# Kernel optimization log

Measured on AMD Instinct MI355X. Metric: run time of the kernel, lower is better.

## Reference

```python
import jax, jax.numpy as jnp
import numpy as np

N_NODES = 50000
N_EDGES = 600000
NUM_RELS = 5
IN_CH = 768
HID = 128
OUT_CH = 128
REL_DIM = 200


def _segment_softmax(scores, seg, n):
    # numerically stable softmax over variable-size segments (destination nodes)
    m = jax.ops.segment_max(scores, seg, num_segments=n)
    e = jnp.exp(scores - m[seg])
    s = jax.ops.segment_sum(e, seg, num_segments=n)
    return e / s[seg]


def _hgn_conv(x, edge_index, edge_type, W, Wr, a, Wres, rel_tab, final):
    # x: [N, h_in]; W: [h, h_in]; Wr: [h, rel_dim]; a: [3h]; rel_tab: [R, rel_dim]
    src = edge_index[0]
    dst = edge_index[1]
    n = x.shape[0]
    h = W.shape[0]
    Wx = x @ W.T                      # [N, h] (shared by x_i, x_j, messages)
    rel = rel_tab[edge_type] @ Wr.T   # [E, h]
    aA, aB, aC = a[:h], a[h:2 * h], a[2 * h:]
    # a([Wx_i | Wx_j | Wr rel]) decomposed to avoid materializing the concat
    score = Wx[dst] @ aA + Wx[src] @ aB + rel @ aC   # [E]
    alpha = jax.nn.leaky_relu(score, 0.2)
    alpha = _segment_softmax(alpha, dst, n)
    agg = jax.ops.segment_sum(Wx[src] * alpha[:, None], dst, num_segments=n)
    out = jax.nn.elu(agg + x @ Wres.T)
    if final:
        out = out / jnp.maximum(jnp.linalg.norm(out, axis=1, keepdims=True), 1e-12)
    return out, alpha


def setup_inputs() -> dict:
    key = jax.random.key(0)
    ks = jax.random.split(key, 20)
    s = 0.02
    return {
        "x": jax.random.normal(ks[0], (N_NODES, IN_CH), jnp.float32),
        "edge_index": jax.random.randint(ks[1], (2, N_EDGES), 0, N_NODES, jnp.int64 if jax.config.jax_enable_x64 else jnp.int32),
        "edge_type": jax.random.randint(ks[2], (N_EDGES,), 0, NUM_RELS, jnp.int64 if jax.config.jax_enable_x64 else jnp.int32),
        "l1_W": jax.random.normal(ks[3], (HID, IN_CH), jnp.float32) * s,
        "l1_b": jnp.zeros((HID,), jnp.float32),
        "l2_W": jax.random.normal(ks[4], (OUT_CH, HID), jnp.float32) * s,
        "l2_b": jnp.zeros((OUT_CH,), jnp.float32),
        "W1": jax.random.normal(ks[5], (HID, HID), jnp.float32) * s,
        "Wr1": jax.random.normal(ks[6], (HID, REL_DIM), jnp.float32) * s,
        "a1": jax.random.normal(ks[7], (3 * HID,), jnp.float32) * s,
        "Wres1": jax.random.normal(ks[8], (HID, HID), jnp.float32) * s,
        "rel1": jax.random.normal(ks[9], (NUM_RELS, REL_DIM), jnp.float32),
        "W2": jax.random.normal(ks[10], (HID, HID), jnp.float32) * s,
        "Wr2": jax.random.normal(ks[11], (HID, REL_DIM), jnp.float32) * s,
        "a2": jax.random.normal(ks[12], (3 * HID,), jnp.float32) * s,
        "Wres2": jax.random.normal(ks[13], (HID, HID), jnp.float32) * s,
        "rel2": jax.random.normal(ks[14], (NUM_RELS, REL_DIM), jnp.float32),
    }


def reference(x, edge_index, edge_type, l1_W, l1_b, l2_W, l2_b,
              W1, Wr1, a1, Wres1, rel1, W2, Wr2, a2, Wres2, rel2):
    out = jax.nn.leaky_relu(x @ l1_W.T + l1_b, 0.01)
    # layer 1 (dropout is identity in eval mode)
    out, alpha = _hgn_conv(out, edge_index, edge_type, W1, Wr1, a1, Wres1, rel1, final=False)
    # layer 2: original code blends alpha into self.alpha but weights messages
    # with its own (unblended) softmax alpha, so pre_alpha does not affect output
    out, _ = _hgn_conv(out, edge_index, edge_type, W2, Wr2, a2, Wres2, rel2, final=True)
    out = jax.nn.leaky_relu(out @ l2_W.T + l2_b, 0.01)
    return out
```

## Files before the change

### kernel.cpp

```cpp
#include <hip/hip_runtime.h>

namespace {

typedef unsigned short ushort_t;
typedef unsigned int uint_t;
typedef __attribute__((ext_vector_type(8))) short bf16x8;
typedef __attribute__((ext_vector_type(4))) float f32x4;

constexpr int N   = 50000;
constexpr int E   = 600000;
constexpr int NR  = 5;
constexpr int KIN = 768;
constexpr int H   = 128;
constexpr int RD  = 200;

__device__ inline ushort_t f2b(float f){
  uint_t u = __builtin_bit_cast(uint_t, f);
  uint_t r = (u + 0x7FFFu + ((u >> 16) & 1u)) >> 16;
  return (ushort_t)r;
}
__device__ inline float b2f_lo(uint_t u){ return __builtin_bit_cast(float, u << 16); }
__device__ inline float b2f_hi(uint_t u){ return __builtin_bit_cast(float, u & 0xFFFF0000u); }

__global__ void cvt_all_k(const float* __restrict__ l1W, const float* __restrict__ W1,
                          const float* __restrict__ R1, const float* __restrict__ W2,
                          const float* __restrict__ R2, const float* __restrict__ l2W,
                          ushort_t* __restrict__ dst){
  constexpr int S0 = H * KIN;
  constexpr int S1 = H * H;
  int i = blockIdx.x * 256 + threadIdx.x;
  if (i >= S0 + 5 * S1) return;
  float v;
  if (i < S0) v = l1W[i];
  else {
    int j = i - S0, seg = j >> 14, off = j & (S1 - 1);
    const float* srcs[5] = {W1, R1, W2, R2, l2W};
    v = srcs[seg][off];
  }
  dst[i] = f2b(v);
}

__global__ void relsc_k(const float* __restrict__ rel1, const float* __restrict__ Wr1,
                        const float* __restrict__ a1, float* __restrict__ sC1,
                        const float* __restrict__ rel2, const float* __restrict__ Wr2,
                        const float* __restrict__ a2, float* __restrict__ sC2){
  const float* rel = blockIdx.x ? rel2 : rel1;
  const float* Wr  = blockIdx.x ? Wr2  : Wr1;
  const float* a   = blockIdx.x ? a2   : a1;
  float*       sC  = blockIdx.x ? sC2  : sC1;
  __shared__ float red[128];
  int n = threadIdx.x;
  float aC = a[256 + n];
  for (int r = 0; r < NR; ++r){
    float p = 0.f;
    for (int k = 0; k < RD; ++k) p += rel[r * RD + k] * Wr[n * RD + k];
    red[n] = p * aC;
    __syncthreads();
    for (int s = 64; s > 0; s >>= 1){
      if (n < s) red[n] += red[n + s];
      __syncthreads();
    }
    if (n == 0) sC[r] = red[0];
    __syncthreads();
  }
}

template<int K, int MODE, bool AFP32, bool OUTBF, bool NORM>
__global__ __launch_bounds__(256) void mgemm_k(const void* __restrict__ Ap,
    const ushort_t* __restrict__ Wb, const float* __restrict__ avec,
    const float* __restrict__ aggM, void* __restrict__ outp,
    float* __restrict__ sA, float* __restrict__ sB, int M)
{
  constexpr int AP = 40;
  constexpr int BP = 40;
  __shared__ __align__(16) ushort_t As[64 * AP];
  __shared__ __align__(16) ushort_t Bs[128 * BP];
  const int tid  = threadIdx.x;
  const int wave = tid >> 6, lane = tid & 63;
  const int l15  = lane & 15, quad = lane >> 4;
  const int row0 = blockIdx.x * 64;

  f32x4 acc[8];
  #pragma unroll
  for (int t = 0; t < 8; ++t) acc[t] = (f32x4){0.f, 0.f, 0.f, 0.f};

  for (int k0 = 0; k0 < K; k0 += 32){
    {
      int r = tid >> 2, q = tid & 3;
      int grow = row0 + r;
      ushort_t v[8] = {0,0,0,0,0,0,0,0};
      if (grow < M){
        if (AFP32){
          const float* ap = (const float*)Ap + (size_t)grow * K + k0 + q * 8;
          float4 u0 = *reinterpret_cast<const float4*>(ap);
          float4 u1 = *reinterpret_cast<const float4*>(ap + 4);
          v[0]=f2b(u0.x); v[1]=f2b(u0.y); v[2]=f2b(u0.z); v[3]=f2b(u0.w);
          v[4]=f2b(u1.x); v[5]=f2b(u1.y); v[6]=f2b(u1.z); v[7]=f2b(u1.w);
        } else {
          const uint4 u = *reinterpret_cast<const uint4*>(
              (const ushort_t*)Ap + (size_t)grow * K + k0 + q * 8);
          *reinterpret_cast<uint4*>(v) = u;
        }
      }
      *reinterpret_cast<uint4*>(&As[r * AP + q * 8]) = *reinterpret_cast<uint4*>(v);
    }
    {
      int n = tid >> 1, seg = tid & 1;
      const ushort_t* wp = Wb + (size_t)n * K + k0 + seg * 16;
      uint4 v0 = *reinterpret_cast<const uint4*>(wp);
      uint4 v1 = *reinterpret_cast<const uint4*>(wp + 8);
      *reinterpret_cast<uint4*>(&Bs[n * BP + seg * 16])     = v0;
      *reinterpret_cast<uint4*>(&Bs[n * BP + seg * 16 + 8]) = v1;
    }
    __syncthreads();
    bf16x8 af = *reinterpret_cast<const bf16x8*>(&As[(wave * 16 + l15) * AP + quad * 8]);
    #pragma unroll
    for (int t = 0; t < 8; ++t){
      bf16x8 bf = *reinterpret_cast<const bf16x8*>(&Bs[(t * 16 + l15) * BP + quad * 8]);
      acc[t] = __builtin_amdgcn_mfma_f32_16x16x32_bf16(af, bf, acc[t], 0, 0, 0);
    }
    __syncthreads();
  }

  float vv[8][4];
  #pragma unroll
  for (int t = 0; t < 8; ++t){
    #pragma unroll
    for (int r = 0; r < 4; ++r){
      int grow = row0 + wave * 16 + quad * 4 + r;
      int col  = t * 16 + l15;
      float v = acc[t][r];
      if (MODE == 1){
        v += avec[col];
        v = v > 0.f ? v : 0.01f * v;
      } else if (MODE == 2){
        if (grow < M) v += aggM[(size_t)grow * 128 + col];
        v = v > 0.f ? v : __expf(v) - 1.f;
      }
      vv[t][r] = v;
    }
  }

  if (MODE == 3){
    #pragma unroll
    for (int r = 0; r < 4; ++r){
      float pa = 0.f, pb = 0.f;
      #pragma unroll
      for (int t = 0; t < 8; ++t){
        int col = t * 16 + l15;
        pa += vv[t][r] * avec[col];
        pb += vv[t][r] * avec[128 + col];
      }
      #pragma unroll
      for (int off = 1; off < 16; off <<= 1){
        pa += __shfl_xor(pa, off, 64);
        pb += __shfl_xor(pb, off, 64);
      }
      int grow = row0 + wave * 16 + quad * 4 + r;
      if (l15 == r && grow < M){ sA[grow] = pa; sB[grow] = pb; }
    }
  }

  if (NORM){
    #pragma unroll
    for (int r = 0; r < 4; ++r){
      float ss = 0.f;
      #pragma unroll
      for (int t = 0; t < 8; ++t) ss += vv[t][r] * vv[t][r];
      #pragma unroll
      for (int off = 1; off < 16; off <<= 1) ss += __shfl_xor(ss, off, 64);
      float sc = 1.f / fmaxf(sqrtf(ss), 1e-12f);
      #pragma unroll
      for (int t = 0; t < 8; ++t) vv[t][r] *= sc;
    }
  }

  #pragma unroll
  for (int t = 0; t < 8; ++t){
    #pragma unroll
    for (int r = 0; r < 4; ++r){
      int grow = row0 + wave * 16 + quad * 4 + r;
      if (grow >= M) continue;
      int col = t * 16 + l15;
      if (OUTBF) ((ushort_t*)outp)[(size_t)grow * 128 + col] = f2b(vv[t][r]);
      else       ((float*)outp)   [(size_t)grow * 128 + col] = vv[t][r];
    }
  }
}

__global__ void degcount_k(const int* __restrict__ dst, int* __restrict__ deg){
  int e = blockIdx.x * 256 + threadIdx.x;
  if (e < E) atomicAdd(&deg[dst[e]], 1);
}

__global__ void scan1_k(const int* __restrict__ deg, int* __restrict__ chunk,
                        int* __restrict__ bsums, int n){
  __shared__ int s[256];
  int tid = threadIdx.x, i = blockIdx.x * 256 + tid;
  int v = (i < n) ? deg[i] : 0;
  s[tid] = v; __syncthreads();
  for (int off = 1; off < 256; off <<= 1){
    int t = (tid >= off) ? s[tid - off] : 0;
    __syncthreads();
    s[tid] += t;
    __syncthreads();
  }
  if (i < n) chunk[i] = s[tid] - v;
  if (tid == 255) bsums[blockIdx.x] = s[255];
}

__global__ void scan2_k(const int* __restrict__ bsums, int* __restrict__ boffs, int nb){
  __shared__ int s[256];
  int tid = threadIdx.x;
  int v = (tid < nb) ? bsums[tid] : 0;
  s[tid] = v; __syncthreads();
  for (int off = 1; off < 256; off <<= 1){
    int t = (tid >= off) ? s[tid - off] : 0;
    __syncthreads();
    s[tid] += t;
    __syncthreads();
  }
  if (tid < nb) boffs[tid] = s[tid] - v;
}

__global__ void scan3_k(int* __restrict__ rowptr, const int* __restrict__ boffs,
                        int* __restrict__ cursor, int n, int total){
  int i = blockIdx.x * 256 + threadIdx.x;
  if (i < n){
    int v = rowptr[i] + boffs[blockIdx.x];
    rowptr[i] = v; cursor[i] = v;
  }
  if (i == 0) rowptr[n] = total;
}

__global__ void fill_k(const int* __restrict__ src, const int* __restrict__ dst,
                       const int* __restrict__ et, int* __restrict__ cursor,
                       int* __restrict__ csrc, int* __restrict__ ctype){
  int e = blockIdx.x * 256 + threadIdx.x;
  if (e < E){
    int d = dst[e];
    int p = atomicAdd(&cursor[d], 1);
    csrc[p]  = src[e];
    ctype[p] = et[e];
  }
}

__global__ void agg_k(const ushort_t* __restrict__ Wx, const float* __restrict__ sA,
                      const float* __restrict__ sB, const float* __restrict__ sC,
                      const int* __restrict__ rowptr, const int* __restrict__ csrc,
                      const int* __restrict__ ctype, float* __restrict__ agg, int n){
  int node = blockIdx.x * 4 + (threadIdx.x >> 6);
  int lane = threadIdx.x & 63;
  if (node >= n) return;
  int p0 = rowptr[node], p1 = rowptr[node + 1];
  int deg = p1 - p0;
  float sa = sA[node];
  float m = -1e30f, ssum = 0.f, a0 = 0.f, a1 = 0.f;

  for (int c0 = 0; c0 < deg; c0 += 64){
    int cnt = deg - c0; if (cnt > 64) cnt = 64;
    bool ok = lane < cnt;
    int p = p0 + c0 + (ok ? lane : 0);
    int sn = csrc[p];
    int tp = ctype[p];
    float s = sa + sB[sn] + sC[tp];
    s = s > 0.f ? s : 0.2f * s;
    float sv = ok ? s : -1e30f;
    #pragma unroll
    for (int off = 32; off > 0; off >>= 1) sv = fmaxf(sv, __shfl_xor(sv, off, 64));
    float mn = fmaxf(m, sv);
    float corr = __expf(m - mn);
    ssum *= corr; a0 *= corr; a1 *= corr;
    float ev = ok ? __expf(s - mn) : 0.f;
    float es = ev;
    #pragma unroll
    for (int off = 32; off > 0; off >>= 1) es += __shfl_xor(es, off, 64);
    ssum += es;
    int sng = ok ? sn : 0;
    m = mn;

    for (int e = 0; e < cnt; e += 4){
      int  n0 = __shfl(sng, e,     64), n1 = __shfl(sng, e + 1, 64);
      int  n2 = __shfl(sng, e + 2, 64), n3 = __shfl(sng, e + 3, 64);
      float e0 = __shfl(ev, e,     64), e1 = __shfl(ev, e + 1, 64);
      float e2 = __shfl(ev, e + 2, 64), e3 = __shfl(ev, e + 3, 64);
      uint_t u0 = *reinterpret_cast<const uint_t*>(Wx + (size_t)n0 * 128 + lane * 2);
      uint_t u1 = *reinterpret_cast<const uint_t*>(Wx + (size_t)n1 * 128 + lane * 2);
      uint_t u2 = *reinterpret_cast<const uint_t*>(Wx + (size_t)n2 * 128 + lane * 2);
      uint_t u3 = *reinterpret_cast<const uint_t*>(Wx + (size_t)n3 * 128 + lane * 2);
      a0 += e0 * b2f_lo(u0); a1 += e0 * b2f_hi(u0);
      a0 += e1 * b2f_lo(u1); a1 += e1 * b2f_hi(u1);
      a0 += e2 * b2f_lo(u2); a1 += e2 * b2f_hi(u2);
      a0 += e3 * b2f_lo(u3); a1 += e3 * b2f_hi(u3);
    }
  }
  float inv = (deg > 0) ? 1.f / ssum : 0.f;
  float2 w; w.x = a0 * inv; w.y = a1 * inv;
  *reinterpret_cast<float2*>(agg + (size_t)node * 128 + lane * 2) = w;
}

}

extern "C" void kernel_launch(void* const* d_in, const int* in_sizes, int n_in,
                              void* d_out, int out_size, void* d_ws, size_t ws_size,
                              hipStream_t stream)
{
  const float* x     = (const float*)d_in[0];
  const int*   eidx  = (const int*)d_in[1];
  const int*   et    = (const int*)d_in[2];
  const float* l1W   = (const float*)d_in[3];
  const float* l1b   = (const float*)d_in[4];
  const float* l2W   = (const float*)d_in[5];
  const float* l2b   = (const float*)d_in[6];
  const float* W1    = (const float*)d_in[7];
  const float* Wr1   = (const float*)d_in[8];
  const float* a1    = (const float*)d_in[9];
  const float* Wres1 = (const float*)d_in[10];
  const float* rel1  = (const float*)d_in[11];
  const float* W2    = (const float*)d_in[12];
  const float* Wr2   = (const float*)d_in[13];
  const float* a2    = (const float*)d_in[14];
  const float* Wres2 = (const float*)d_in[15];
  const float* rel2  = (const float*)d_in[16];
  float* outp = (float*)d_out;

  const int* esrc = eidx;
  const int* edst = eidx + E;

  float* f = (float*)d_ws;
  size_t o = 0;
  float* aggF = f + o; o += (size_t)N * H;
  float* sA   = f + o; o += N;
  float* sB   = f + o; o += N;
  float* sC1  = f + o; o += 8;
  float* sC2  = f + o; o += 8;
  ushort_t* us = (ushort_t*)(f + o);
  size_t ou = 0;
  ushort_t* b0   = us + ou; ou += (size_t)N * H;
  ushort_t* b1   = us + ou; ou += (size_t)N * H;
  ushort_t* Wxb  = us + ou; ou += (size_t)N * H;
  ushort_t* wtsb = us + ou; ou += (size_t)H * KIN + 5 * H * H;
  ushort_t* l1Wb = wtsb;
  ushort_t* W1b  = wtsb + H * KIN;
  ushort_t* R1b  = W1b + H * H;
  ushort_t* W2b  = R1b + H * H;
  ushort_t* R2b  = W2b + H * H;
  ushort_t* l2Wb = R2b + H * H;
  if (ou & 1) ou += 1;
  int* wi = (int*)(us + ou);
  size_t oi = 0;
  int* deg    = wi + oi; oi += N;
  int* rowptr = wi + oi; oi += N + 1;
  int* cursor = wi + oi; oi += N;
  int* bsums  = wi + oi; oi += 256;
  int* boffs  = wi + oi; oi += 256;
  int* csrc   = wi + oi; oi += E;
  int* ctype  = wi + oi; oi += E;

  const int EB    = (E + 255) / 256;
  const int NB256 = (N + 255) / 256;
  const int GB    = (N + 63) / 64;
  const int NB4   = (N + 3) / 4;
  const int CVB   = (H * KIN + 5 * H * H + 255) / 256;

  hipMemsetAsync(deg, 0, sizeof(int) * N, stream);
  degcount_k<<<EB, 256, 0, stream>>>(edst, deg);
  scan1_k<<<NB256, 256, 0, stream>>>(deg, rowptr, bsums, N);
  scan2_k<<<1, 256, 0, stream>>>(bsums, boffs, NB256);
  scan3_k<<<NB256, 256, 0, stream>>>(rowptr, boffs, cursor, N, E);
  fill_k<<<EB, 256, 0, stream>>>(esrc, edst, et, cursor, csrc, ctype);

  cvt_all_k<<<CVB, 256, 0, stream>>>(l1W, W1, Wres1, W2, Wres2, l2W, wtsb);
  relsc_k<<<2, 128, 0, stream>>>(rel1, Wr1, a1, sC1, rel2, Wr2, a2, sC2);

  mgemm_k<KIN, 1, true, true, false><<<GB, 256, 0, stream>>>(
      x, l1Wb, l1b, nullptr, b0, nullptr, nullptr, N);

  mgemm_k<H, 3, false, true, false><<<GB, 256, 0, stream>>>(
      b0, W1b, a1, nullptr, Wxb, sA, sB, N);
  agg_k<<<NB4, 256, 0, stream>>>(Wxb, sA, sB, sC1, rowptr, csrc, ctype, aggF, N);
  mgemm_k<H, 2, false, true, false><<<GB, 256, 0, stream>>>(
      b0, R1b, nullptr, aggF, b1, nullptr, nullptr, N);

  mgemm_k<H, 3, false, true, false><<<GB, 256, 0, stream>>>(
      b1, W2b, a2, nullptr, Wxb, sA, sB, N);
  agg_k<<<NB4, 256, 0, stream>>>(Wxb, sA, sB, sC2, rowptr, csrc, ctype, aggF, N);
  mgemm_k<H, 2, false, true, true><<<GB, 256, 0, stream>>>(
      b1, R2b, nullptr, aggF, b0, nullptr, nullptr, N);

  mgemm_k<H, 1, false, false, false><<<GB, 256, 0, stream>>>(
      b0, l2Wb, l2b, nullptr, outp, nullptr, nullptr, N);
}
```

Baseline: 529.1 us.

## Fuse consecutive GEMMs per row block, pack edge CSR, bf16 aggregation buffer

Chains each pair of consecutive per-node GEMMs into one kernel: the first GEMM's epilogue output is kept in shared memory as bf16 and fed straight into the second GEMM, so the intermediate no longer needs a global round trip or a separate launch. Edge source and type are packed into one int in the CSR, and the aggregation output becomes bf16 instead of fp32, which cuts memory traffic. The weight conversion, degree zeroing and relation-score setup are merged into one prep kernel. In exchange it uses more shared memory per block, adds extra bf16 rounding of the aggregate, and the 16-bit source packing only works while node ids stay below 65536.

```diff
diff --git a/kernel.cpp b/kernel.cpp
--- a/kernel.cpp
+++ b/kernel.cpp
@@ -21,169 +21,53 @@
 }
 __device__ inline float b2f_lo(uint_t u){ return __builtin_bit_cast(float, u << 16); }
 __device__ inline float b2f_hi(uint_t u){ return __builtin_bit_cast(float, u & 0xFFFF0000u); }
-
-__global__ void cvt_all_k(const float* __restrict__ l1W, const float* __restrict__ W1,
-                          const float* __restrict__ R1, const float* __restrict__ W2,
-                          const float* __restrict__ R2, const float* __restrict__ l2W,
-                          ushort_t* __restrict__ dst){
+__device__ inline float b2f_us(ushort_t h){ return __builtin_bit_cast(float, ((uint_t)h) << 16); }
+
+__global__ void prep_k(const float* __restrict__ l1W, const float* __restrict__ W1,
+                       const float* __restrict__ R1, const float* __restrict__ W2,
+                       const float* __restrict__ R2, const float* __restrict__ l2W,
+                       ushort_t* __restrict__ wts, int* __restrict__ deg,
+                       const float* __restrict__ rel1, const float* __restrict__ Wr1,
+                       const float* __restrict__ a1, float* __restrict__ sC1,
+                       const float* __restrict__ rel2, const float* __restrict__ Wr2,
+                       const float* __restrict__ a2, float* __restrict__ sC2){
   constexpr int S0 = H * KIN;
   constexpr int S1 = H * H;
-  int i = blockIdx.x * 256 + threadIdx.x;
-  if (i >= S0 + 5 * S1) return;
-  float v;
-  if (i < S0) v = l1W[i];
-  else {
-    int j = i - S0, seg = j >> 14, off = j & (S1 - 1);
-    const float* srcs[5] = {W1, R1, W2, R2, l2W};
-    v = srcs[seg][off];
-  }
-  dst[i] = f2b(v);
-}
-
-__global__ void relsc_k(const float* __restrict__ rel1, const float* __restrict__ Wr1,
-                        const float* __restrict__ a1, float* __restrict__ sC1,
-                        const float* __restrict__ rel2, const float* __restrict__ Wr2,
-                        const float* __restrict__ a2, float* __restrict__ sC2){
-  const float* rel = blockIdx.x ? rel2 : rel1;
-  const float* Wr  = blockIdx.x ? Wr2  : Wr1;
-  const float* a   = blockIdx.x ? a2   : a1;
-  float*       sC  = blockIdx.x ? sC2  : sC1;
-  __shared__ float red[128];
-  int n = threadIdx.x;
-  float aC = a[256 + n];
-  for (int r = 0; r < NR; ++r){
-    float p = 0.f;
-    for (int k = 0; k < RD; ++k) p += rel[r * RD + k] * Wr[n * RD + k];
-    red[n] = p * aC;
-    __syncthreads();
-    for (int s = 64; s > 0; s >>= 1){
-      if (n < s) red[n] += red[n + s];
+  int b = blockIdx.x, tid = threadIdx.x;
+  if (b < 704){
+    int i = b * 256 + tid;
+    float v;
+    if (i < S0) v = l1W[i];
+    else {
+      int j = i - S0, seg = j >> 14, off = j & (S1 - 1);
+      const float* srcs[5] = {W1, R1, W2, R2, l2W};
+      v = srcs[seg][off];
+    }
+    wts[i] = f2b(v);
+  } else if (b < 900){
+    int i = (b - 704) * 256 + tid;
+    if (i < N) deg[i] = 0;
+  } else {
+    int L = b - 900;
+    const float* rel = L ? rel2 : rel1;
+    const float* Wr  = L ? Wr2  : Wr1;
+    const float* a   = L ? a2   : a1;
+    float*       sC  = L ? sC2  : sC1;
+    __shared__ float red[256];
+    int n = tid >> 1, half = tid & 1;
+    float aC = a[256 + n];
+    for (int r = 0; r < NR; ++r){
+      float p = 0.f;
+      for (int k = half * 100; k < half * 100 + 100; ++k)
+        p += rel[r * RD + k] * Wr[n * RD + k];
+      red[tid] = p * aC;
       __syncthreads();
-    }
-    if (n == 0) sC[r] = red[0];
-    __syncthreads();
-  }
-}
-
-template<int K, int MODE, bool AFP32, bool OUTBF, bool NORM>
-__global__ __launch_bounds__(256) void mgemm_k(const void* __restrict__ Ap,
-    const ushort_t* __restrict__ Wb, const float* __restrict__ avec,
-    const float* __restrict__ aggM, void* __restrict__ outp,
-    float* __restrict__ sA, float* __restrict__ sB, int M)
-{
-  constexpr int AP = 40;
-  constexpr int BP = 40;
-  __shared__ __align__(16) ushort_t As[64 * AP];
-  __shared__ __align__(16) ushort_t Bs[128 * BP];
-  const int tid  = threadIdx.x;
-  const int wave = tid >> 6, lane = tid & 63;
-  const int l15  = lane & 15, quad = lane >> 4;
-  const int row0 = blockIdx.x * 64;
-
-  f32x4 acc[8];
-  #pragma unroll
-  for (int t = 0; t < 8; ++t) acc[t] = (f32x4){0.f, 0.f, 0.f, 0.f};
-
-  for (int k0 = 0; k0 < K; k0 += 32){
-    {
-      int r = tid >> 2, q = tid & 3;
-      int grow = row0 + r;
-      ushort_t v[8] = {0,0,0,0,0,0,0,0};
-      if (grow < M){
-        if (AFP32){
-          const float* ap = (const float*)Ap + (size_t)grow * K + k0 + q * 8;
-          float4 u0 = *reinterpret_cast<const float4*>(ap);
-          float4 u1 = *reinterpret_cast<const float4*>(ap + 4);
-          v[0]=f2b(u0.x); v[1]=f2b(u0.y); v[2]=f2b(u0.z); v[3]=f2b(u0.w);
-          v[4]=f2b(u1.x); v[5]=f2b(u1.y); v[6]=f2b(u1.z); v[7]=f2b(u1.w);
-        } else {
-          const uint4 u = *reinterpret_cast<const uint4*>(
-              (const ushort_t*)Ap + (size_t)grow * K + k0 + q * 8);
-          *reinterpret_cast<uint4*>(v) = u;
-        }
-      }
-      *reinterpret_cast<uint4*>(&As[r * AP + q * 8]) = *reinterpret_cast<uint4*>(v);
-    }
-    {
-      int n = tid >> 1, seg = tid & 1;
-      const ushort_t* wp = Wb + (size_t)n * K + k0 + seg * 16;
-      uint4 v0 = *reinterpret_cast<const uint4*>(wp);
-      uint4 v1 = *reinterpret_cast<const uint4*>(wp + 8);
-      *reinterpret_cast<uint4*>(&Bs[n * BP + seg * 16])     = v0;
-      *reinterpret_cast<uint4*>(&Bs[n * BP + seg * 16 + 8]) = v1;
-    }
-    __syncthreads();
-    bf16x8 af = *reinterpret_cast<const bf16x8*>(&As[(wave * 16 + l15) * AP + quad * 8]);
-    #pragma unroll
-    for (int t = 0; t < 8; ++t){
-      bf16x8 bf = *reinterpret_cast<const bf16x8*>(&Bs[(t * 16 + l15) * BP + quad * 8]);
-      acc[t] = __builtin_amdgcn_mfma_f32_16x16x32_bf16(af, bf, acc[t], 0, 0, 0);
-    }
-    __syncthreads();
-  }
-
-  float vv[8][4];
-  #pragma unroll
-  for (int t = 0; t < 8; ++t){
-    #pragma unroll
-    for (int r = 0; r < 4; ++r){
-      int grow = row0 + wave * 16 + quad * 4 + r;
-      int col  = t * 16 + l15;
-      float v = acc[t][r];
-      if (MODE == 1){
-        v += avec[col];
-        v = v > 0.f ? v : 0.01f * v;
-      } else if (MODE == 2){
-        if (grow < M) v += aggM[(size_t)grow * 128 + col];
-        v = v > 0.f ? v : __expf(v) - 1.f;
-      }
-      vv[t][r] = v;
-    }
-  }
-
-  if (MODE == 3){
-    #pragma unroll
-    for (int r = 0; r < 4; ++r){
-      float pa = 0.f, pb = 0.f;
-      #pragma unroll
-      for (int t = 0; t < 8; ++t){
-        int col = t * 16 + l15;
-        pa += vv[t][r] * avec[col];
-        pb += vv[t][r] * avec[128 + col];
-      }
-      #pragma unroll
-      for (int off = 1; off < 16; off <<= 1){
-        pa += __shfl_xor(pa, off, 64);
-        pb += __shfl_xor(pb, off, 64);
-      }
-      int grow = row0 + wave * 16 + quad * 4 + r;
-      if (l15 == r && grow < M){ sA[grow] = pa; sB[grow] = pb; }
-    }
-  }
-
-  if (NORM){
-    #pragma unroll
-    for (int r = 0; r < 4; ++r){
-      float ss = 0.f;
-      #pragma unroll
-      for (int t = 0; t < 8; ++t) ss += vv[t][r] * vv[t][r];
-      #pragma unroll
-      for (int off = 1; off < 16; off <<= 1) ss += __shfl_xor(ss, off, 64);
-      float sc = 1.f / fmaxf(sqrtf(ss), 1e-12f);
-      #pragma unroll
-      for (int t = 0; t < 8; ++t) vv[t][r] *= sc;
-    }
-  }
-
-  #pragma unroll
-  for (int t = 0; t < 8; ++t){
-    #pragma unroll
-    for (int r = 0; r < 4; ++r){
-      int grow = row0 + wave * 16 + quad * 4 + r;
-      if (grow >= M) continue;
-      int col = t * 16 + l15;
-      if (OUTBF) ((ushort_t*)outp)[(size_t)grow * 128 + col] = f2b(vv[t][r]);
-      else       ((float*)outp)   [(size_t)grow * 128 + col] = vv[t][r];
+      for (int s = 128; s > 0; s >>= 1){
+        if (tid < s) red[tid] += red[tid + s];
+        __syncthreads();
+      }
+      if (tid == 0) sC[r] = red[0];
+      __syncthreads();
     }
   }
 }
@@ -235,20 +119,202 @@
 
 __global__ void fill_k(const int* __restrict__ src, const int* __restrict__ dst,
                        const int* __restrict__ et, int* __restrict__ cursor,
-                       int* __restrict__ csrc, int* __restrict__ ctype){
+                       int* __restrict__ cpk){
   int e = blockIdx.x * 256 + threadIdx.x;
   if (e < E){
     int d = dst[e];
     int p = atomicAdd(&cursor[d], 1);
-    csrc[p]  = src[e];
-    ctype[p] = et[e];
+    cpk[p] = src[e] | (et[e] << 16);
+  }
+}
+
+template<int K1, int M1, bool AFP32, bool NORM, bool STORE1, int M2>
+__global__ __launch_bounds__(256) void gfused_k(
+    const void* __restrict__ Ap, const ushort_t* __restrict__ Wb1,
+    const float* __restrict__ bias1, const ushort_t* __restrict__ aggM,
+    ushort_t* __restrict__ out1,
+    const ushort_t* __restrict__ Wb2, const float* __restrict__ vec2,
+    void* __restrict__ out2, float* __restrict__ sA, float* __restrict__ sB, int M)
+{
+  constexpr int AP = 40;
+  constexpr int BP = 40;
+  constexpr int CP = 136;
+  __shared__ __align__(16) ushort_t As[64 * AP];
+  __shared__ __align__(16) ushort_t Bs[128 * BP];
+  __shared__ __align__(16) ushort_t Cs[64 * CP];
+  const int tid  = threadIdx.x;
+  const int wave = tid >> 6, lane = tid & 63;
+  const int l15  = lane & 15, quad = lane >> 4;
+  const int row0 = blockIdx.x * 64;
+
+  if (M1 == 2){
+    #pragma unroll
+    for (int i = 0; i < 4; ++i){
+      int idx = tid + 256 * i;
+      int r = idx >> 4, c8 = idx & 15;
+      int grow = row0 + r;
+      uint4 v = make_uint4(0, 0, 0, 0);
+      if (grow < M) v = *reinterpret_cast<const uint4*>(aggM + (size_t)grow * 128 + c8 * 8);
+      *reinterpret_cast<uint4*>(&Cs[r * CP + c8 * 8]) = v;
+    }
+  }
+
+  f32x4 acc[8];
+  #pragma unroll
+  for (int t = 0; t < 8; ++t) acc[t] = (f32x4){0.f, 0.f, 0.f, 0.f};
+
+  for (int k0 = 0; k0 < K1; k0 += 32){
+    {
+      int r = tid >> 2, q = tid & 3;
+      int grow = row0 + r;
+      ushort_t v[8] = {0,0,0,0,0,0,0,0};
+      if (grow < M){
+        if (AFP32){
+          const float* ap = (const float*)Ap + (size_t)grow * K1 + k0 + q * 8;
+          float4 u0 = *reinterpret_cast<const float4*>(ap);
+          float4 u1 = *reinterpret_cast<const float4*>(ap + 4);
+          v[0]=f2b(u0.x); v[1]=f2b(u0.y); v[2]=f2b(u0.z); v[3]=f2b(u0.w);
+          v[4]=f2b(u1.x); v[5]=f2b(u1.y); v[6]=f2b(u1.z); v[7]=f2b(u1.w);
+        } else {
+          const uint4 u = *reinterpret_cast<const uint4*>(
+              (const ushort_t*)Ap + (size_t)grow * K1 + k0 + q * 8);
+          *reinterpret_cast<uint4*>(v) = u;
+        }
+      }
+      *reinterpret_cast<uint4*>(&As[r * AP + q * 8]) = *reinterpret_cast<uint4*>(v);
+    }
+    {
+      int n = tid >> 1, seg = tid & 1;
+      const ushort_t* wp = Wb1 + (size_t)n * K1 + k0 + seg * 16;
+      uint4 v0 = *reinterpret_cast<const uint4*>(wp);
+      uint4 v1 = *reinterpret_cast<const uint4*>(wp + 8);
+      *reinterpret_cast<uint4*>(&Bs[n * BP + seg * 16])     = v0;
+      *reinterpret_cast<uint4*>(&Bs[n * BP + seg * 16 + 8]) = v1;
+    }
+    __syncthreads();
+    bf16x8 af = *reinterpret_cast<const bf16x8*>(&As[(wave * 16 + l15) * AP + quad * 8]);
+    #pragma unroll
+    for (int t = 0; t < 8; ++t){
+      bf16x8 bfr = *reinterpret_cast<const bf16x8*>(&Bs[(t * 16 + l15) * BP + quad * 8]);
+      acc[t] = __builtin_amdgcn_mfma_f32_16x16x32_bf16(af, bfr, acc[t], 0, 0, 0);
+    }
+    __syncthreads();
+  }
+
+  float vv[8][4];
+  #pragma unroll
+  for (int t = 0; t < 8; ++t){
+    #pragma unroll
+    for (int r = 0; r < 4; ++r){
+      int lr  = wave * 16 + quad * 4 + r;
+      int col = t * 16 + l15;
+      float v = acc[t][r];
+      if (M1 == 1){
+        v += bias1[col];
+        v = v > 0.f ? v : 0.01f * v;
+      } else {
+        v += b2f_us(Cs[lr * CP + col]);
+        v = v > 0.f ? v : __expf(v) - 1.f;
+      }
+      vv[t][r] = v;
+    }
+  }
+  if (NORM){
+    #pragma unroll
+    for (int r = 0; r < 4; ++r){
+      float ss = 0.f;
+      #pragma unroll
+      for (int t = 0; t < 8; ++t) ss += vv[t][r] * vv[t][r];
+      #pragma unroll
+      for (int off = 1; off < 16; off <<= 1) ss += __shfl_xor(ss, off, 64);
+      float sc = 1.f / fmaxf(sqrtf(ss), 1e-12f);
+      #pragma unroll
+      for (int t = 0; t < 8; ++t) vv[t][r] *= sc;
+    }
+  }
+  #pragma unroll
+  for (int t = 0; t < 8; ++t){
+    #pragma unroll
+    for (int r = 0; r < 4; ++r){
+      int lr  = wave * 16 + quad * 4 + r;
+      int col = t * 16 + l15;
+      int grow = row0 + lr;
+      ushort_t h = f2b(vv[t][r]);
+      if (STORE1 && grow < M) out1[(size_t)grow * 128 + col] = h;
+      Cs[lr * CP + col] = h;
+    }
+  }
+  __syncthreads();
+
+  #pragma unroll
+  for (int t = 0; t < 8; ++t) acc[t] = (f32x4){0.f, 0.f, 0.f, 0.f};
+  for (int k0 = 0; k0 < 128; k0 += 32){
+    {
+      int n = tid >> 1, seg = tid & 1;
+      const ushort_t* wp = Wb2 + (size_t)n * 128 + k0 + seg * 16;
+      uint4 v0 = *reinterpret_cast<const uint4*>(wp);
+      uint4 v1 = *reinterpret_cast<const uint4*>(wp + 8);
+      *reinterpret_cast<uint4*>(&Bs[n * BP + seg * 16])     = v0;
+      *reinterpret_cast<uint4*>(&Bs[n * BP + seg * 16 + 8]) = v1;
+    }
+    __syncthreads();
+    bf16x8 af = *reinterpret_cast<const bf16x8*>(&Cs[(wave * 16 + l15) * CP + k0 + quad * 8]);
+    #pragma unroll
+    for (int t = 0; t < 8; ++t){
+      bf16x8 bfr = *reinterpret_cast<const bf16x8*>(&Bs[(t * 16 + l15) * BP + quad * 8]);
+      acc[t] = __builtin_amdgcn_mfma_f32_16x16x32_bf16(af, bfr, acc[t], 0, 0, 0);
+    }
+    __syncthreads();
+  }
+
+  if (M2 == 1){
+    #pragma unroll
+    for (int t = 0; t < 8; ++t){
+      #pragma unroll
+      for (int r = 0; r < 4; ++r){
+        int grow = row0 + wave * 16 + quad * 4 + r;
+        if (grow >= M) continue;
+        int col = t * 16 + l15;
+        float v = acc[t][r] + vec2[col];
+        v = v > 0.f ? v : 0.01f * v;
+        ((float*)out2)[(size_t)grow * 128 + col] = v;
+      }
+    }
+  } else {
+    #pragma unroll
+    for (int t = 0; t < 8; ++t){
+      #pragma unroll
+      for (int r = 0; r < 4; ++r){
+        int grow = row0 + wave * 16 + quad * 4 + r;
+        if (grow >= M) continue;
+        int col = t * 16 + l15;
+        ((ushort_t*)out2)[(size_t)grow * 128 + col] = f2b(acc[t][r]);
+      }
+    }
+    #pragma unroll
+    for (int r = 0; r < 4; ++r){
+      float pa = 0.f, pb = 0.f;
+      #pragma unroll
+      for (int t = 0; t < 8; ++t){
+        int col = t * 16 + l15;
+        pa += acc[t][r] * vec2[col];
+        pb += acc[t][r] * vec2[128 + col];
+      }
+      #pragma unroll
+      for (int off = 1; off < 16; off <<= 1){
+        pa += __shfl_xor(pa, off, 64);
+        pb += __shfl_xor(pb, off, 64);
+      }
+      int grow = row0 + wave * 16 + quad * 4 + r;
+      if (l15 == r && grow < M){ sA[grow] = pa; sB[grow] = pb; }
+    }
   }
 }
 
 __global__ void agg_k(const ushort_t* __restrict__ Wx, const float* __restrict__ sA,
                       const float* __restrict__ sB, const float* __restrict__ sC,
-                      const int* __restrict__ rowptr, const int* __restrict__ csrc,
-                      const int* __restrict__ ctype, float* __restrict__ agg, int n){
+                      const int* __restrict__ rowptr, const int* __restrict__ cpk,
+                      uint_t* __restrict__ aggU, int n){
   int node = blockIdx.x * 4 + (threadIdx.x >> 6);
   int lane = threadIdx.x & 63;
   if (node >= n) return;
@@ -260,10 +326,10 @@
   for (int c0 = 0; c0 < deg; c0 += 64){
     int cnt = deg - c0; if (cnt > 64) cnt = 64;
     bool ok = lane < cnt;
-    int p = p0 + c0 + (ok ? lane : 0);
-    int sn = csrc[p];
-    int tp = ctype[p];
-    float s = sa + sB[sn] + sC[tp];
+    int p  = p0 + c0 + (ok ? lane : 0);
+    int pk = cpk[p];
+    int sn = pk & 0xFFFF;
+    float s = sa + sB[sn] + sC[pk >> 16];
     s = s > 0.f ? s : 0.2f * s;
     float sv = ok ? s : -1e30f;
     #pragma unroll
@@ -276,12 +342,12 @@
     #pragma unroll
     for (int off = 32; off > 0; off >>= 1) es += __shfl_xor(es, off, 64);
     ssum += es;
-    int sng = ok ? sn : 0;
+    int png = ok ? pk : 0;
     m = mn;
 
     for (int e = 0; e < cnt; e += 4){
-      int  n0 = __shfl(sng, e,     64), n1 = __shfl(sng, e + 1, 64);
-      int  n2 = __shfl(sng, e + 2, 64), n3 = __shfl(sng, e + 3, 64);
+      int  n0 = __shfl(png, e,     64) & 0xFFFF, n1 = __shfl(png, e + 1, 64) & 0xFFFF;
+      int  n2 = __shfl(png, e + 2, 64) & 0xFFFF, n3 = __shfl(png, e + 3, 64) & 0xFFFF;
       float e0 = __shfl(ev, e,     64), e1 = __shfl(ev, e + 1, 64);
       float e2 = __shfl(ev, e + 2, 64), e3 = __shfl(ev, e + 3, 64);
       uint_t u0 = *reinterpret_cast<const uint_t*>(Wx + (size_t)n0 * 128 + lane * 2);
@@ -295,8 +361,8 @@
     }
   }
   float inv = (deg > 0) ? 1.f / ssum : 0.f;
-  float2 w; w.x = a0 * inv; w.y = a1 * inv;
-  *reinterpret_cast<float2*>(agg + (size_t)node * 128 + lane * 2) = w;
+  uint_t o = (uint_t)f2b(a0 * inv) | ((uint_t)f2b(a1 * inv) << 16);
+  aggU[(size_t)node * 64 + lane] = o;
 }
 
 }
@@ -329,7 +395,6 @@
 
   float* f = (float*)d_ws;
   size_t o = 0;
-  float* aggF = f + o; o += (size_t)N * H;
   float* sA   = f + o; o += N;
   float* sB   = f + o; o += N;
   float* sC1  = f + o; o += 8;
@@ -339,6 +404,7 @@
   ushort_t* b0   = us + ou; ou += (size_t)N * H;
   ushort_t* b1   = us + ou; ou += (size_t)N * H;
   ushort_t* Wxb  = us + ou; ou += (size_t)N * H;
+  ushort_t* aggB = us + ou; ou += (size_t)N * H;
   ushort_t* wtsb = us + ou; ou += (size_t)H * KIN + 5 * H * H;
   ushort_t* l1Wb = wtsb;
   ushort_t* W1b  = wtsb + H * KIN;
@@ -354,40 +420,29 @@
   int* cursor = wi + oi; oi += N;
   int* bsums  = wi + oi; oi += 256;
   int* boffs  = wi + oi; oi += 256;
-  int* csrc   = wi + oi; oi += E;
-  int* ctype  = wi + oi; oi += E;
+  int* cpk    = wi + oi; oi += E;
 
   const int EB    = (E + 255) / 256;
   const int NB256 = (N + 255) / 256;
   const int GB    = (N + 63) / 64;
   const int NB4   = (N + 3) / 4;
-  const int CVB   = (H * KIN + 5 * H * H + 255) / 256;
-
-  hipMemsetAsync(deg, 0, sizeof(int) * N, stream);
+
+  prep_k<<<902, 256, 0, stream>>>(l1W, W1, Wres1, W2, Wres2, l2W, wtsb, deg,
+                                  rel1, Wr1, a1, sC1, rel2, Wr2, a2, sC2);
   degcount_k<<<EB, 256, 0, stream>>>(edst, deg);
   scan1_k<<<NB256, 256, 0, stream>>>(deg, rowptr, bsums, N);
   scan2_k<<<1, 256, 0, stream>>>(bsums, boffs, NB256);
   scan3_k<<<NB256, 256, 0, stream>>>(rowptr, boffs, cursor, N, E);
-  fill_k<<<EB, 256, 0, stream>>>(esrc, edst, et, cursor, csrc, ctype);
-
-  cvt_all_k<<<CVB, 256, 0, stream>>>(l1W, W1, Wres1, W2, Wres2, l2W, wtsb);
-  relsc_k<<<2, 128, 0, stream>>>(rel1, Wr1, a1, sC1, rel2, Wr2, a2, sC2);
-
-  mgemm_k<KIN, 1, true, true, false><<<GB, 256, 0, stream>>>(
-      x, l1Wb, l1b, nullptr, b0, nullptr, nullptr, N);
-
-  mgemm_k<H, 3, false, true, false><<<GB, 256, 0, stream>>>(
-      b0, W1b, a1, nullptr, Wxb, sA, sB, N);
-  agg_k<<<NB4, 256, 0, stream>>>(Wxb, sA, sB, sC1, rowptr, csrc, ctype, aggF, N);
-  mgemm_k<H, 2, false, true, false><<<GB, 256, 0, stream>>>(
-      b0, R1b, nullptr, aggF, b1, nullptr, nullptr, N);
-
-  mgemm_k<H, 3, false, true, false><<<GB, 256, 0, stream>>>(
-      b1, W2b, a2, nullptr, Wxb, sA, sB, N);
-  agg_k<<<NB4, 256, 0, stream>>>(Wxb, sA, sB, sC2, rowptr, csrc, ctype, aggF, N);
-  mgemm_k<H, 2, false, true, true><<<GB, 256, 0, stream>>>(
-      b1, R2b, nullptr, aggF, b0, nullptr, nullptr, N);
-
-  mgemm_k<H, 1, false, false, false><<<GB, 256, 0, stream>>>(
-      b0, l2Wb, l2b, nullptr, outp, nullptr, nullptr, N);
-}
+  fill_k<<<EB, 256, 0, stream>>>(esrc, edst, et, cursor, cpk);
+
+  gfused_k<KIN, 1, true, false, true, 3><<<GB, 256, 0, stream>>>(
+      x, l1Wb, l1b, nullptr, b0, W1b, a1, Wxb, sA, sB, N);
+  agg_k<<<NB4, 256, 0, stream>>>(Wxb, sA, sB, sC1, rowptr, cpk, (uint_t*)aggB, N);
+
+  gfused_k<H, 2, false, false, true, 3><<<GB, 256, 0, stream>>>(
+      b0, R1b, nullptr, aggB, b1, W2b, a2, Wxb, sA, sB, N);
+  agg_k<<<NB4, 256, 0, stream>>>(Wxb, sA, sB, sC2, rowptr, cpk, (uint_t*)aggB, N);
+
+  gfused_k<H, 2, false, true, false, 1><<<GB, 256, 0, stream>>>(
+      b1, R2b, nullptr, aggB, nullptr, l2Wb, l2b, outp, nullptr, nullptr, N);
+}
```

New measurement: 480.9 us. 9.1% less time.
